# Kernel tuning notes

Hardware: AMD Instinct MI355X
Metric: run time of the kernel (lower is better)

## Reference

```python
import jax, jax.numpy as jnp
import numpy as np

B, S, SE, D, H = 4, 1024, 256, 1536, 24
HD = D // H
EPS = 1e-5
STYLE_IDX = np.array([0, 0, 2, 2])  # expand_first: style stats of sample 0 -> {0,1}, sample 2 -> {2,3}


def adain(feat):
    # feat: [B,H,S,hd]; stats over seq dim (-2), unbiased var like torch
    m = feat.mean(axis=-2, keepdims=True)
    s = jnp.sqrt(feat.var(axis=-2, keepdims=True, ddof=1) + EPS)
    sm, ss = m[STYLE_IDX], s[STYLE_IDX]
    styled = (feat - m) / s * ss + sm
    # only batch indices 1 and 3 are restyled
    mask = jnp.array([0.0, 1.0, 0.0, 1.0], dtype=feat.dtype).reshape(B, 1, 1, 1)
    return feat * (1.0 - mask) + styled * mask


def heads(x):
    b, s, _ = x.shape
    return x.reshape(b, s, H, HD).transpose(0, 2, 1, 3)


def setup_inputs() -> dict:
    key = jax.random.key(0)
    ks = jax.random.split(key, 12)
    w = lambda k: jax.random.normal(k, (D, D), dtype=jnp.float32) * 0.02
    z = jnp.zeros((D,), dtype=jnp.float32)
    return {
        'hidden_states': jax.random.normal(ks[0], (B, S, D), dtype=jnp.float32),
        'encoder_hidden_states': jax.random.normal(ks[1], (B, SE, D), dtype=jnp.float32),
        'wq': w(ks[2]), 'bq': z, 'wk': w(ks[3]), 'bk': z, 'wv': w(ks[4]), 'bv': z,
        'awq': w(ks[5]), 'abq': z, 'awk': w(ks[6]), 'abk': z, 'awv': w(ks[7]), 'abv': z,
        'wo': w(ks[8]), 'bo': z, 'wao': w(ks[9]), 'bao': z,
    }


def reference(hidden_states, encoder_hidden_states, wq, bq, wk, bk, wv, bv,
              awq, abq, awk, abk, awv, abv, wo, bo, wao, bao):
    q = heads(hidden_states @ wq + bq)   # [B,H,S,hd]
    k = heads(hidden_states @ wk + bk)
    v = heads(hidden_states @ wv + bv)
    # adain_queries / adain_keys (adain_values=False)
    q = adain(q)
    k = adain(k)
    # share_attention: concat style K/V (scale=1.0 -> plain expand) along seq
    k = jnp.concatenate([k, k[STYLE_IDX]], axis=2)  # [B,H,2S,hd]
    v = jnp.concatenate([v, v[STYLE_IDX]], axis=2)
    # joint (text) streams
    eq = heads(encoder_hidden_states @ awq + abq)
    ek = heads(encoder_hidden_states @ awk + abk)
    ev = heads(encoder_hidden_states @ awv + abv)
    q = jnp.concatenate([q, eq], axis=2)   # [B,H,S+SE,hd]
    k = jnp.concatenate([k, ek], axis=2)   # [B,H,2S+SE,hd]
    v = jnp.concatenate([v, ev], axis=2)
    scale = 1.0 / np.sqrt(HD)
    logits = jnp.einsum('bhqd,bhkd->bhqk', q, k) * scale
    probs = jax.nn.softmax(logits, axis=-1)
    out = jnp.einsum('bhqk,bhkd->bhqd', probs, v)
    out = out.transpose(0, 2, 1, 3).reshape(B, -1, D)
    hid, enc = out[:, :S], out[:, S:]
    hid = hid @ wo + bo            # to_out[0] (to_out[1] is dropout/identity)
    enc = enc @ wao + bao          # to_add_out (context_pre_only=False)
    return hid, enc
```

## Files before the change

### kernel.cpp

```cpp
#include <hip/hip_runtime.h>
#include <hip/hip_bf16.h>


#define NB 4
#define NS 1024
#define NSE 256
#define ND 1536
#define NH 24
#define LK2 1280
#define SMAX 20.0f
#define LOG2E 1.44269504f

typedef short bf16x8 __attribute__((ext_vector_type(8)));
typedef float f32x4 __attribute__((ext_vector_type(4)));

struct WPtrs { const float* w[8]; };
struct B6    { const float* p[6]; };

__device__ __forceinline__ unsigned short f2bf(float x) {
  union { float f; unsigned u; } a; a.f = x;
  unsigned r = a.u + 0x7fffu + ((a.u >> 16) & 1u);
  return (unsigned short)(r >> 16);
}
__device__ __forceinline__ void split2(float x, unsigned short& h, unsigned short& l) {
  union { float f; unsigned u; } a; a.f = x;
  h = (unsigned short)(a.u >> 16);
  union { float f; unsigned u; } b; b.u = a.u & 0xffff0000u;
  union { float f; unsigned u; } c; c.f = x - b.f;
  l = (unsigned short)(c.u >> 16);
}

__device__ __forceinline__ void gload_lds16(const unsigned short* g, unsigned short* l) {
  __builtin_amdgcn_global_load_lds(
      (const __attribute__((address_space(1))) void*)g,
      (__attribute__((address_space(3))) void*)l, 16, 0, 0);
}

__global__ __launch_bounds__(256) void conv_split_all(
    const float* __restrict__ hs, const float* __restrict__ ehs,
    unsigned short* __restrict__ HSh, unsigned short* __restrict__ HSl,
    unsigned short* __restrict__ EHh, unsigned short* __restrict__ EHl)
{
  int i = blockIdx.x * 256 + threadIdx.x;
  const float4* src; ushort4 *dh, *dl; int j;
  if (i < 1572864) { src = (const float4*)hs; j = i; dh = (ushort4*)HSh; dl = (ushort4*)HSl; }
  else { j = i - 1572864; src = (const float4*)ehs; dh = (ushort4*)EHh; dl = (ushort4*)EHl; }
  float4 v = src[j];
  ushort4 h, lo;
  split2(v.x, h.x, lo.x); split2(v.y, h.y, lo.y);
  split2(v.z, h.z, lo.z); split2(v.w, h.w, lo.w);
  dh[j] = h; dl[j] = lo;
}

__global__ __launch_bounds__(256) void conv_wt_all(WPtrs wp,
                                                   unsigned short* __restrict__ Wsp)
{
  __shared__ float tile[32][33];
  const int z = blockIdx.z;
  const float* W = wp.w[z];
  unsigned short* Th = Wsp + (long)(2 * z) * 2359296;
  unsigned short* Tl = Th + 2359296;
  const int k0 = blockIdx.x * 32, n0 = blockIdx.y * 32;
  const int r = threadIdx.x >> 5, c = threadIdx.x & 31;
#pragma unroll
  for (int i = 0; i < 4; ++i)
    tile[r + 8 * i][c] = W[(long)(k0 + r + 8 * i) * ND + n0 + c];
  __syncthreads();
#pragma unroll
  for (int i = 0; i < 4; ++i) {
    float v = tile[c][r + 8 * i];
    long o = (long)(n0 + r + 8 * i) * ND + k0 + c;
    unsigned short h, l;
    split2(v, h, l);
    Th[o] = h; Tl[o] = l;
  }
}

__device__ __forceinline__ void gemm_mfma_body(
    const unsigned short* __restrict__ Ah, const unsigned short* __restrict__ Al,
    const unsigned short* __restrict__ Bh, const unsigned short* __restrict__ Bl,
    const float* __restrict__ bias, float* __restrict__ C, int m0, int n0,
    bool third)
{
  __shared__ unsigned short sAh[128 * 32], sAl[128 * 32];
  __shared__ unsigned short sBh[128 * 32], sBl[128 * 32];

  const int t = threadIdx.x;
  const int w = t >> 6, l = t & 63;

  const int lr = l >> 2;
  const int lc = (l & 3) * 8;

  const unsigned short* pAh = Ah + (long)(m0 + 32 * w + lr) * ND + lc;
  const unsigned short* pAl = Al + (long)(m0 + 32 * w + lr) * ND + lc;
  const unsigned short* pBh = Bh + (long)(n0 + 32 * w + lr) * ND + lc;
  const unsigned short* pBl = Bl + (long)(n0 + 32 * w + lr) * ND + lc;

  unsigned short* qAh0 = &sAh[(32 * w) * 32];
  unsigned short* qAh1 = &sAh[(32 * w + 16) * 32];
  unsigned short* qAl0 = &sAl[(32 * w) * 32];
  unsigned short* qAl1 = &sAl[(32 * w + 16) * 32];
  unsigned short* qBh0 = &sBh[(32 * w) * 32];
  unsigned short* qBh1 = &sBh[(32 * w + 16) * 32];
  unsigned short* qBl0 = &sBl[(32 * w) * 32];
  unsigned short* qBl1 = &sBl[(32 * w + 16) * 32];

  const int rowA = (w >> 1) * 64 + (l & 15);
  const int rowB = (w & 1) * 64 + (l & 15);
  const int ko = (l >> 4) * 8;

  f32x4 acc[4][4] = {};

  for (int k0 = 0; k0 < ND; k0 += 32) {
    gload_lds16(pAh, qAh0);
    gload_lds16(pAh + 16 * ND, qAh1);
    if (third) {
      gload_lds16(pAl, qAl0);
      gload_lds16(pAl + 16 * ND, qAl1);
    }
    gload_lds16(pBh, qBh0);
    gload_lds16(pBh + 16 * ND, qBh1);
    gload_lds16(pBl, qBl0);
    gload_lds16(pBl + 16 * ND, qBl1);
    pAh += 32; pAl += 32; pBh += 32; pBl += 32;
    __syncthreads();

    bf16x8 fah[4], fal[4], fbh[4], fbl[4];
#pragma unroll
    for (int mt = 0; mt < 4; ++mt)
      fah[mt] = *(const bf16x8*)&sAh[(rowA + mt * 16) * 32 + ko];
    if (third) {
#pragma unroll
      for (int mt = 0; mt < 4; ++mt)
        fal[mt] = *(const bf16x8*)&sAl[(rowA + mt * 16) * 32 + ko];
    }
#pragma unroll
    for (int nt = 0; nt < 4; ++nt) {
      fbh[nt] = *(const bf16x8*)&sBh[(rowB + nt * 16) * 32 + ko];
      fbl[nt] = *(const bf16x8*)&sBl[(rowB + nt * 16) * 32 + ko];
    }
#pragma unroll
    for (int mt = 0; mt < 4; ++mt)
#pragma unroll
      for (int nt = 0; nt < 4; ++nt) {
        acc[mt][nt] = __builtin_amdgcn_mfma_f32_16x16x32_bf16(fah[mt], fbh[nt], acc[mt][nt], 0, 0, 0);
        acc[mt][nt] = __builtin_amdgcn_mfma_f32_16x16x32_bf16(fah[mt], fbl[nt], acc[mt][nt], 0, 0, 0);
      }
    if (third) {
#pragma unroll
      for (int mt = 0; mt < 4; ++mt)
#pragma unroll
        for (int nt = 0; nt < 4; ++nt)
          acc[mt][nt] = __builtin_amdgcn_mfma_f32_16x16x32_bf16(fal[mt], fbh[nt], acc[mt][nt], 0, 0, 0);
    }
    __syncthreads();
  }

  const int col0 = n0 + (w & 1) * 64 + (l & 15);
  const int row0 = m0 + (w >> 1) * 64 + (l >> 4) * 4;
#pragma unroll
  for (int nt = 0; nt < 4; ++nt) {
    float bv = bias[col0 + nt * 16];
#pragma unroll
    for (int mt = 0; mt < 4; ++mt)
#pragma unroll
      for (int r = 0; r < 4; ++r)
        C[(long)(row0 + mt * 16 + r) * ND + col0 + nt * 16] = acc[mt][nt][r] + bv;
  }
}

__global__ __launch_bounds__(256) void gemm3_all(
    const unsigned short* __restrict__ HSh, const unsigned short* __restrict__ HSl,
    const unsigned short* __restrict__ EHh, const unsigned short* __restrict__ EHl,
    const unsigned short* __restrict__ Wsp, B6 biases,
    float* __restrict__ Qb, float* __restrict__ EQb)
{
  const int z = blockIdx.z, y = blockIdx.y;
  const unsigned short *Ah, *Al;
  float* C;
  int m0, widx;
  if (y < 32) { Ah = HSh; Al = HSl; m0 = y * 128; widx = z;
                C = Qb + (long)z * 6291456; }
  else        { Ah = EHh; Al = EHl; m0 = (y - 32) * 128; widx = 3 + z;
                C = EQb + (long)z * 1572864; }
  const unsigned short* Bh = Wsp + (long)(2 * widx) * 2359296;
  const unsigned short* Bl = Bh + 2359296;
  gemm_mfma_body(Ah, Al, Bh, Bl, biases.p[widx], C, m0, blockIdx.x * 128,
                 z == 2);
}

__global__ __launch_bounds__(256) void gemm_out_all(
    const unsigned short* __restrict__ AOh,
    const unsigned short* __restrict__ Wsp,
    const float* __restrict__ bo, const float* __restrict__ bao,
    float* __restrict__ out)
{
  const int z = blockIdx.z, y = blockIdx.y;
  const unsigned short *Ah, *Bh, *Bl;
  const float* bias;
  float* C;
  int m0;
  if (y < 8) {
    Ah = AOh + (long)z * 1966080;
    m0 = y * 128;
    Bh = Wsp + (long)12 * 2359296; Bl = Bh + 2359296;
    bias = bo; C = out + (long)z * 1572864;
  } else {
    Ah = AOh + 1572864 + (long)z * 1966080;
    m0 = (y - 8) * 128;
    Bh = Wsp + (long)14 * 2359296; Bl = Bh + 2359296;
    bias = bao; C = out + 6291456 + (long)z * 393216;
  }
  gemm_mfma_body(Ah, Ah, Bh, Bl, bias, C, m0, blockIdx.x * 128, false);
}

__global__ __launch_bounds__(256) void adain_stats2(
    const float* __restrict__ Qb, const float* __restrict__ Kb,
    float* __restrict__ stm, float* __restrict__ sts,
    float* __restrict__ stm2, float* __restrict__ sts2)
{
  const float* X = blockIdx.z ? Kb : Qb;
  float* meanb = blockIdx.z ? stm2 : stm;
  float* sigb  = blockIdx.z ? sts2 : sts;
  const int b  = blockIdx.x;
  const int t  = threadIdx.x;
  const int dl = t & 63;
  const int sg = t >> 6;
  const int d  = blockIdx.y * 64 + dl;
  const float* xp = X + (long)b * NS * ND + d;
  float sum = 0.f, sq = 0.f;
  for (int s = sg; s < NS; s += 4) {
    float v = xp[(long)s * ND];
    sum += v; sq += v * v;
  }
  __shared__ float ss[4][64], s2[4][64];
  ss[sg][dl] = sum; s2[sg][dl] = sq;
  __syncthreads();
  if (t < 64) {
    float tot = ss[0][t] + ss[1][t] + ss[2][t] + ss[3][t];
    float tq  = s2[0][t] + s2[1][t] + s2[2][t] + s2[3][t];
    float mean = tot * (1.f / 1024.f);
    float var  = (tq - tot * mean) * (1.f / 1023.f);
    meanb[b * ND + blockIdx.y * 64 + t] = mean;
    sigb [b * ND + blockIdx.y * 64 + t] = sqrtf(var + 1e-5f);
  }
}

__global__ __launch_bounds__(256) void conv_KV(
    const float* __restrict__ Kf, const float* __restrict__ EKf,
    const float* __restrict__ Vf, const float* __restrict__ EVf,
    const float* __restrict__ stm2, const float* __restrict__ sts2,
    unsigned short* __restrict__ Kh, unsigned short* __restrict__ Kl,
    unsigned short* __restrict__ VT)
{
  __shared__ float tile[64][65];
  const int bh = blockIdx.y, b = bh / NH, h = bh - b * NH;
  if (blockIdx.x < 20) {
    const int key = blockIdx.x * 64 + (threadIdx.x >> 2);
    const int dc = (threadIdx.x & 3) * 16;
    const bool kad = ((b & 1) != 0) && (key < NS);
    const int srcb = b & 2;
    const float* src = (key < NS)
        ? Kf  + ((long)b * NS + key) * ND + h * 64 + dc
        : EKf + ((long)b * NSE + key - NS) * ND + h * 64 + dc;
    unsigned short* dh = Kh + ((long)bh * LK2 + key) * 64 + dc;
    unsigned short* dl = Kl + ((long)bh * LK2 + key) * 64 + dc;
    const long sb = (long)b * ND + h * 64 + dc;
    const long ss = (long)srcb * ND + h * 64 + dc;
#pragma unroll
    for (int i = 0; i < 4; ++i) {
      float4 v = *(const float4*)(src + 4 * i);
      if (kad) {
        float4 mb = *(const float4*)(stm2 + sb + 4 * i);
        float4 gb = *(const float4*)(sts2 + sb + 4 * i);
        float4 ms = *(const float4*)(stm2 + ss + 4 * i);
        float4 gs = *(const float4*)(sts2 + ss + 4 * i);
        v.x = (v.x - mb.x) * (gs.x / gb.x) + ms.x;
        v.y = (v.y - mb.y) * (gs.y / gb.y) + ms.y;
        v.z = (v.z - mb.z) * (gs.z / gb.z) + ms.z;
        v.w = (v.w - mb.w) * (gs.w / gb.w) + ms.w;
      }
      ushort4 hi, lo;
      split2(v.x, hi.x, lo.x); split2(v.y, hi.y, lo.y);
      split2(v.z, hi.z, lo.z); split2(v.w, hi.w, lo.w);
      *(ushort4*)(dh + 4 * i) = hi;
      *(ushort4*)(dl + 4 * i) = lo;
    }
  } else {
    const int k0 = (blockIdx.x - 20) * 64;
    {
      const int kl_ = threadIdx.x >> 2, dc = (threadIdx.x & 3) * 16;
      const int key = k0 + kl_;
      const float* src = (key < NS)
          ? Vf  + ((long)b * NS + key) * ND + h * 64 + dc
          : EVf + ((long)b * NSE + key - NS) * ND + h * 64 + dc;
#pragma unroll
      for (int i = 0; i < 4; ++i) {
        float4 v = *(const float4*)(src + 4 * i);
        tile[kl_][dc + 4 * i + 0] = v.x; tile[kl_][dc + 4 * i + 1] = v.y;
        tile[kl_][dc + 4 * i + 2] = v.z; tile[kl_][dc + 4 * i + 3] = v.w;
      }
    }
    __syncthreads();
    const int d = threadIdx.x >> 2, kc = (threadIdx.x & 3) * 16;
    unsigned short* dst = VT + ((long)bh * 64 + d) * LK2 + k0 + kc;
#pragma unroll
    for (int i = 0; i < 4; ++i) {
      ushort4 o4;
      o4.x = f2bf(tile[kc + 4 * i + 0][d]);
      o4.y = f2bf(tile[kc + 4 * i + 1][d]);
      o4.z = f2bf(tile[kc + 4 * i + 2][d]);
      o4.w = f2bf(tile[kc + 4 * i + 3][d]);
      *(ushort4*)(dst + 4 * i) = o4;
    }
  }
}

__global__ __launch_bounds__(256) void attn_mfma(
    const float* __restrict__ Q, const float* __restrict__ EQ,
    const unsigned short* __restrict__ Khg, const unsigned short* __restrict__ Klg,
    const unsigned short* __restrict__ VTg,
    const float* __restrict__ stm, const float* __restrict__ sts,
    unsigned short* __restrict__ AOh)
{
  __shared__ unsigned short sKh[2][64 * 64], sKl[2][64 * 64], sVT[2][64 * 64];
  __shared__ unsigned short sPh[64 * 72], sPl[64 * 72];

  const int t = threadIdx.x, w = t >> 6, l = t & 63;
  const int lin = blockIdx.x;
  const int x = lin & 7;
  const int j = lin >> 3;
  const int parity = j & 1;
  const int u = j >> 1;
  const int i6 = 6 * x + u / 20;
  const int q0 = (u % 20) * 64;
  const int bh = parity ? (i6 < 24 ? i6 + 24 : i6 + 48)
                        : (i6 < 24 ? i6      : i6 + 24);
  const int b = bh / NH, h = bh - b * NH;
  const int bhs = (b & 2) * NH + h;
  const int m = l & 15, g = l >> 4;
  const bool beven = (b & 1) == 0;
  const int nIter = beven ? 20 : 36;

  union FU { bf16x8 v; unsigned short u[8]; };
  FU qh[2], ql[2];
  {
    const bool qad = !beven && (q0 < NS);
    const int srcb = b & 2;
    const float* qrow = (q0 < NS)
        ? (Q  + ((long)b * NS + q0 + 16 * w + m) * ND + h * 64)
        : (EQ + ((long)b * NSE + (q0 - NS) + 16 * w + m) * ND + h * 64);
#pragma unroll
    for (int ks = 0; ks < 2; ++ks) {
      const int d0 = h * 64 + ks * 32 + g * 8;
      const float* p = qrow + ks * 32 + g * 8;
      float4 v0 = *(const float4*)p, v1 = *(const float4*)(p + 4);
      float vv[8] = {v0.x, v0.y, v0.z, v0.w, v1.x, v1.y, v1.z, v1.w};
      if (qad) {
        float4 mb0 = *(const float4*)(stm + (long)b * ND + d0);
        float4 mb1 = *(const float4*)(stm + (long)b * ND + d0 + 4);
        float4 gb0 = *(const float4*)(sts + (long)b * ND + d0);
        float4 gb1 = *(const float4*)(sts + (long)b * ND + d0 + 4);
        float4 ms0 = *(const float4*)(stm + (long)srcb * ND + d0);
        float4 ms1 = *(const float4*)(stm + (long)srcb * ND + d0 + 4);
        float4 gs0 = *(const float4*)(sts + (long)srcb * ND + d0);
        float4 gs1 = *(const float4*)(sts + (long)srcb * ND + d0 + 4);
        float mb[8] = {mb0.x, mb0.y, mb0.z, mb0.w, mb1.x, mb1.y, mb1.z, mb1.w};
        float gb[8] = {gb0.x, gb0.y, gb0.z, gb0.w, gb1.x, gb1.y, gb1.z, gb1.w};
        float ms[8] = {ms0.x, ms0.y, ms0.z, ms0.w, ms1.x, ms1.y, ms1.z, ms1.w};
        float gs[8] = {gs0.x, gs0.y, gs0.z, gs0.w, gs1.x, gs1.y, gs1.z, gs1.w};
#pragma unroll
        for (int j2 = 0; j2 < 8; ++j2)
          vv[j2] = (vv[j2] - mb[j2]) * (gs[j2] / gb[j2]) + ms[j2];
      }
#pragma unroll
      for (int j2 = 0; j2 < 8; ++j2)
        split2(vv[j2] * (0.125f * LOG2E), qh[ks].u[j2], ql[ks].u[j2]);
    }
  }

  const int srow = l >> 3;
  const int sp = l & 7;
  const int osw = (sp - srow) & 7;
  const long ownK = (long)bh * LK2 * 64, styK = (long)bhs * LK2 * 64;
  const long ownV = (long)bh * 64 * LK2, styV = (long)bhs * 64 * LK2;
  const int offK = (16 * w + srow) * 64 + osw * 8;
  const int offV = (16 * w + srow) * LK2 + osw * 8;

  auto stage = [&](int kt, int bi) {
    int zone, jz;
    if (beven) { zone = (kt < 16) ? 0 : 2; jz = (kt < 16) ? kt : kt - 16; }
    else {
      zone = (kt < 16) ? 0 : ((kt < 32) ? 1 : 2);
      jz = (kt < 16) ? kt : ((kt < 32) ? kt - 16 : kt - 32);
    }
    const long keyBase = ((zone == 2) ? 1024 : 0) + (long)jz * 64;
    const unsigned short* kb = Khg + ((zone == 1) ? styK : ownK) + keyBase * 64;
    const unsigned short* lb = Klg + ((zone == 1) ? styK : ownK) + keyBase * 64;
    const unsigned short* vb = VTg + ((zone == 1) ? styV : ownV) + keyBase;
    gload_lds16(kb + offK, &sKh[bi][(16 * w) * 64]);
    gload_lds16(kb + 8 * 64 + offK, &sKh[bi][(16 * w + 8) * 64]);
    gload_lds16(lb + offK, &sKl[bi][(16 * w) * 64]);
    gload_lds16(lb + 8 * 64 + offK, &sKl[bi][(16 * w + 8) * 64]);
    gload_lds16(vb + offV, &sVT[bi][(16 * w) * 64]);
    gload_lds16(vb + 8 * LK2 + offV, &sVT[bi][(16 * w + 8) * 64]);
  };

  const int p0 = (g + m) & 7;
  const int p1 = (4 + g + m) & 7;

  f32x4 oacc[4] = {};
  float l_part[4] = {0.f, 0.f, 0.f, 0.f};

  stage(0, 0);

  for (int kt = 0; kt < nIter; ++kt) {
    const int cur = kt & 1;
    __syncthreads();
    if (kt + 1 < nIter) stage(kt + 1, cur ^ 1);

    const float ebias = (beven && kt < 16) ? (1.0f - SMAX * LOG2E)
                                           : (-SMAX * LOG2E);

    f32x4 sacc[4] = {};
    __builtin_amdgcn_s_setprio(1);
#pragma unroll
    for (int ks = 0; ks < 2; ++ks) {
      const int pp = ks ? p1 : p0;
#pragma unroll
      for (int nt = 0; nt < 4; ++nt) {
        const int ak = (nt * 16 + m) * 64 + pp * 8;
        bf16x8 fkh = *(const bf16x8*)&sKh[cur][ak];
        bf16x8 fkl = *(const bf16x8*)&sKl[cur][ak];
        sacc[nt] = __builtin_amdgcn_mfma_f32_16x16x32_bf16(qh[ks].v, fkh, sacc[nt], 0, 0, 0);
        sacc[nt] = __builtin_amdgcn_mfma_f32_16x16x32_bf16(qh[ks].v, fkl, sacc[nt], 0, 0, 0);
        sacc[nt] = __builtin_amdgcn_mfma_f32_16x16x32_bf16(ql[ks].v, fkh, sacc[nt], 0, 0, 0);
      }
    }
    __builtin_amdgcn_s_setprio(0);

#pragma unroll
    for (int nt = 0; nt < 4; ++nt)
#pragma unroll
      for (int r = 0; r < 4; ++r)
        sacc[nt][r] = __builtin_amdgcn_exp2f(sacc[nt][r] + ebias);
#pragma unroll
    for (int r = 0; r < 4; ++r)
      l_part[r] += (sacc[0][r] + sacc[1][r]) + (sacc[2][r] + sacc[3][r]);
#pragma unroll
    for (int nt = 0; nt < 4; ++nt)
#pragma unroll
      for (int r = 0; r < 4; ++r) {
        unsigned short ph, pl;
        split2(sacc[nt][r], ph, pl);
        const int ad = (16 * w + 4 * g + r) * 72 + nt * 16 + m;
        sPh[ad] = ph; sPl[ad] = pl;
      }

    __builtin_amdgcn_s_setprio(1);
#pragma unroll
    for (int ks = 0; ks < 2; ++ks) {
      const int pp = ks ? p1 : p0;
      const int ap = (16 * w + m) * 72 + ks * 32 + g * 8;
      bf16x8 fph = *(const bf16x8*)&sPh[ap];
      bf16x8 fpl = *(const bf16x8*)&sPl[ap];
#pragma unroll
      for (int nt2 = 0; nt2 < 4; ++nt2) {
        const int av = (nt2 * 16 + m) * 64 + pp * 8;
        bf16x8 fv = *(const bf16x8*)&sVT[cur][av];
        oacc[nt2] = __builtin_amdgcn_mfma_f32_16x16x32_bf16(fph, fv, oacc[nt2], 0, 0, 0);
        oacc[nt2] = __builtin_amdgcn_mfma_f32_16x16x32_bf16(fpl, fv, oacc[nt2], 0, 0, 0);
      }
    }
    __builtin_amdgcn_s_setprio(0);
  }

#pragma unroll
  for (int r = 0; r < 4; ++r) {
#pragma unroll
    for (int off = 1; off < 16; off <<= 1)
      l_part[r] += __shfl_xor(l_part[r], off, 16);
  }
#pragma unroll
  for (int r = 0; r < 4; ++r) {
    float inv = 1.f / l_part[r];
    const long row = (long)b * 1280 + q0 + 16 * w + 4 * g + r;
    const long base = row * ND + h * 64;
#pragma unroll
    for (int nt2 = 0; nt2 < 4; ++nt2)
      AOh[base + nt2 * 16 + m] = f2bf(oacc[nt2][r] * inv);
  }
}

extern "C" void kernel_launch(void* const* d_in, const int* in_sizes, int n_in,
                              void* d_out, int out_size, void* d_ws, size_t ws_size,
                              hipStream_t stream) {
  const float* hs  = (const float*)d_in[0];
  const float* ehs = (const float*)d_in[1];
  WPtrs wp;
  wp.w[0] = (const float*)d_in[2];  wp.w[1] = (const float*)d_in[4];
  wp.w[2] = (const float*)d_in[6];  wp.w[3] = (const float*)d_in[8];
  wp.w[4] = (const float*)d_in[10]; wp.w[5] = (const float*)d_in[12];
  wp.w[6] = (const float*)d_in[14]; wp.w[7] = (const float*)d_in[16];
  B6 biases;
  biases.p[0] = (const float*)d_in[3];
  biases.p[1] = (const float*)d_in[5];
  biases.p[2] = (const float*)d_in[7];
  biases.p[3] = (const float*)d_in[9];
  biases.p[4] = (const float*)d_in[11];
  biases.p[5] = (const float*)d_in[13];
  const float* bo  = (const float*)d_in[15];
  const float* bao = (const float*)d_in[17];
  float* out = (float*)d_out;

  float* Qb  = (float*)d_ws;
  float* Kb  = Qb  + 6291456;
  float* Vb  = Kb  + 6291456;
  float* EQb = Vb  + 6291456;
  float* EKb = EQb + 1572864;
  float* EVb = EKb + 1572864;
  float* stm  = EVb + 1572864;
  float* sts  = stm + 6144;
  float* stm2 = sts + 6144;
  float* sts2 = stm2 + 6144;
  unsigned short* U0  = (unsigned short*)(sts2 + 6144);
  unsigned short* HSh = U0;
  unsigned short* HSl = U0 + 6291456;
  unsigned short* EHh = U0 + 12582912;
  unsigned short* EHl = U0 + 14155776;
  unsigned short* AOh = U0;
  unsigned short* Wsp = U0 + 15728640;
  unsigned short* Khg = Wsp;
  unsigned short* Klg = Wsp + 7864320;
  unsigned short* VTg = Wsp + 15728640;

  dim3 blk(256);

  conv_split_all<<<7680, blk, 0, stream>>>(hs, ehs, HSh, HSl, EHh, EHl);
  conv_wt_all<<<dim3(48, 48, 8), blk, 0, stream>>>(wp, Wsp);

  gemm3_all<<<dim3(12, 40, 3), blk, 0, stream>>>(
      HSh, HSl, EHh, EHl, Wsp, biases, Qb, EQb);

  adain_stats2<<<dim3(4, 24, 2), blk, 0, stream>>>(Qb, Kb, stm, sts, stm2, sts2);

  conv_KV<<<dim3(40, 96), blk, 0, stream>>>(Kb, EKb, Vb, EVb, stm2, sts2,
                                            Khg, Klg, VTg);

  attn_mfma<<<dim3(1920), blk, 0, stream>>>(Qb, EQb, Khg, Klg, VTg,
                                            stm, sts, AOh);

  gemm_out_all<<<dim3(12, 10, 4), blk, 0, stream>>>(AOh, Wsp, bo, bao, out);
}
```

Baseline: 759.9 us.

## Halve attention key tile, pair even/odd heads per block, raise occupancy

The attention kernel now stages 32-key tiles instead of 64, which roughly halves shared memory per block, and sets launch bounds to 4 blocks per CU to raise occupancy. Each block now processes two (batch, head) segments in turn, one even batch with 40 iterations and one odd batch with 72, so all blocks carry the same amount of work and the grid is halved. A new swizzle for the transposed V tile and a narrower P buffer go with the smaller tile. In exchange there are twice as many iterations and barriers per key range, and less MFMA work between each barrier.

```diff
diff --git a/kernel.cpp b/kernel.cpp
--- a/kernel.cpp
+++ b/kernel.cpp
@@ -316,179 +316,177 @@
   }
 }
 
-__global__ __launch_bounds__(256) void attn_mfma(
+__global__ __launch_bounds__(256, 4) void attn_mfma(
     const float* __restrict__ Q, const float* __restrict__ EQ,
     const unsigned short* __restrict__ Khg, const unsigned short* __restrict__ Klg,
     const unsigned short* __restrict__ VTg,
     const float* __restrict__ stm, const float* __restrict__ sts,
     unsigned short* __restrict__ AOh)
 {
-  __shared__ unsigned short sKh[2][64 * 64], sKl[2][64 * 64], sVT[2][64 * 64];
-  __shared__ unsigned short sPh[64 * 72], sPl[64 * 72];
+  __shared__ unsigned short sKh[2][32 * 64], sKl[2][32 * 64], sVT[2][64 * 32];
+  __shared__ unsigned short sPh[64 * 40], sPl[64 * 40];
 
   const int t = threadIdx.x, w = t >> 6, l = t & 63;
-  const int lin = blockIdx.x;
-  const int x = lin & 7;
-  const int j = lin >> 3;
-  const int parity = j & 1;
-  const int u = j >> 1;
+  const int x = blockIdx.x & 7;
+  const int u = blockIdx.x >> 3;
   const int i6 = 6 * x + u / 20;
   const int q0 = (u % 20) * 64;
-  const int bh = parity ? (i6 < 24 ? i6 + 24 : i6 + 48)
-                        : (i6 < 24 ? i6      : i6 + 24);
-  const int b = bh / NH, h = bh - b * NH;
-  const int bhs = (b & 2) * NH + h;
   const int m = l & 15, g = l >> 4;
-  const bool beven = (b & 1) == 0;
-  const int nIter = beven ? 20 : 36;
-
-  union FU { bf16x8 v; unsigned short u[8]; };
-  FU qh[2], ql[2];
-  {
-    const bool qad = !beven && (q0 < NS);
-    const int srcb = b & 2;
-    const float* qrow = (q0 < NS)
-        ? (Q  + ((long)b * NS + q0 + 16 * w + m) * ND + h * 64)
-        : (EQ + ((long)b * NSE + (q0 - NS) + 16 * w + m) * ND + h * 64);
-#pragma unroll
-    for (int ks = 0; ks < 2; ++ks) {
-      const int d0 = h * 64 + ks * 32 + g * 8;
-      const float* p = qrow + ks * 32 + g * 8;
-      float4 v0 = *(const float4*)p, v1 = *(const float4*)(p + 4);
-      float vv[8] = {v0.x, v0.y, v0.z, v0.w, v1.x, v1.y, v1.z, v1.w};
-      if (qad) {
-        float4 mb0 = *(const float4*)(stm + (long)b * ND + d0);
-        float4 mb1 = *(const float4*)(stm + (long)b * ND + d0 + 4);
-        float4 gb0 = *(const float4*)(sts + (long)b * ND + d0);
-        float4 gb1 = *(const float4*)(sts + (long)b * ND + d0 + 4);
-        float4 ms0 = *(const float4*)(stm + (long)srcb * ND + d0);
-        float4 ms1 = *(const float4*)(stm + (long)srcb * ND + d0 + 4);
-        float4 gs0 = *(const float4*)(sts + (long)srcb * ND + d0);
-        float4 gs1 = *(const float4*)(sts + (long)srcb * ND + d0 + 4);
-        float mb[8] = {mb0.x, mb0.y, mb0.z, mb0.w, mb1.x, mb1.y, mb1.z, mb1.w};
-        float gb[8] = {gb0.x, gb0.y, gb0.z, gb0.w, gb1.x, gb1.y, gb1.z, gb1.w};
-        float ms[8] = {ms0.x, ms0.y, ms0.z, ms0.w, ms1.x, ms1.y, ms1.z, ms1.w};
-        float gs[8] = {gs0.x, gs0.y, gs0.z, gs0.w, gs1.x, gs1.y, gs1.z, gs1.w};
-#pragma unroll
-        for (int j2 = 0; j2 < 8; ++j2)
-          vv[j2] = (vv[j2] - mb[j2]) * (gs[j2] / gb[j2]) + ms[j2];
-      }
-#pragma unroll
-      for (int j2 = 0; j2 < 8; ++j2)
-        split2(vv[j2] * (0.125f * LOG2E), qh[ks].u[j2], ql[ks].u[j2]);
-    }
-  }
-
-  const int srow = l >> 3;
-  const int sp = l & 7;
-  const int osw = (sp - srow) & 7;
-  const long ownK = (long)bh * LK2 * 64, styK = (long)bhs * LK2 * 64;
-  const long ownV = (long)bh * 64 * LK2, styV = (long)bhs * 64 * LK2;
-  const int offK = (16 * w + srow) * 64 + osw * 8;
-  const int offV = (16 * w + srow) * LK2 + osw * 8;
-
-  auto stage = [&](int kt, int bi) {
-    int zone, jz;
-    if (beven) { zone = (kt < 16) ? 0 : 2; jz = (kt < 16) ? kt : kt - 16; }
-    else {
-      zone = (kt < 16) ? 0 : ((kt < 32) ? 1 : 2);
-      jz = (kt < 16) ? kt : ((kt < 32) ? kt - 16 : kt - 32);
-    }
-    const long keyBase = ((zone == 2) ? 1024 : 0) + (long)jz * 64;
-    const unsigned short* kb = Khg + ((zone == 1) ? styK : ownK) + keyBase * 64;
-    const unsigned short* lb = Klg + ((zone == 1) ? styK : ownK) + keyBase * 64;
-    const unsigned short* vb = VTg + ((zone == 1) ? styV : ownV) + keyBase;
-    gload_lds16(kb + offK, &sKh[bi][(16 * w) * 64]);
-    gload_lds16(kb + 8 * 64 + offK, &sKh[bi][(16 * w + 8) * 64]);
-    gload_lds16(lb + offK, &sKl[bi][(16 * w) * 64]);
-    gload_lds16(lb + 8 * 64 + offK, &sKl[bi][(16 * w + 8) * 64]);
-    gload_lds16(vb + offV, &sVT[bi][(16 * w) * 64]);
-    gload_lds16(vb + 8 * LK2 + offV, &sVT[bi][(16 * w + 8) * 64]);
-  };
+
+  const int srow = l >> 3, sp = l & 7;
+  const int offK = (8 * w + srow) * 64 + ((sp - srow) & 7) * 8;
+  const int dv = l >> 2, cv = l & 3;
+  const int vrow = 16 * w + dv;
+  const int vcol = ((cv - ((dv + (dv >> 2)) & 3)) & 3) * 8;
+  const int rfm = (m + (m >> 2)) & 3;
 
   const int p0 = (g + m) & 7;
   const int p1 = (4 + g + m) & 7;
 
-  f32x4 oacc[4] = {};
-  float l_part[4] = {0.f, 0.f, 0.f, 0.f};
-
-  stage(0, 0);
-
-  for (int kt = 0; kt < nIter; ++kt) {
-    const int cur = kt & 1;
-    __syncthreads();
-    if (kt + 1 < nIter) stage(kt + 1, cur ^ 1);
-
-    const float ebias = (beven && kt < 16) ? (1.0f - SMAX * LOG2E)
-                                           : (-SMAX * LOG2E);
-
-    f32x4 sacc[4] = {};
-    __builtin_amdgcn_s_setprio(1);
-#pragma unroll
-    for (int ks = 0; ks < 2; ++ks) {
-      const int pp = ks ? p1 : p0;
-#pragma unroll
-      for (int nt = 0; nt < 4; ++nt) {
-        const int ak = (nt * 16 + m) * 64 + pp * 8;
-        bf16x8 fkh = *(const bf16x8*)&sKh[cur][ak];
-        bf16x8 fkl = *(const bf16x8*)&sKl[cur][ak];
-        sacc[nt] = __builtin_amdgcn_mfma_f32_16x16x32_bf16(qh[ks].v, fkh, sacc[nt], 0, 0, 0);
-        sacc[nt] = __builtin_amdgcn_mfma_f32_16x16x32_bf16(qh[ks].v, fkl, sacc[nt], 0, 0, 0);
-        sacc[nt] = __builtin_amdgcn_mfma_f32_16x16x32_bf16(ql[ks].v, fkh, sacc[nt], 0, 0, 0);
-      }
-    }
-    __builtin_amdgcn_s_setprio(0);
-
-#pragma unroll
-    for (int nt = 0; nt < 4; ++nt)
+  union FU { bf16x8 v; unsigned short u[8]; };
+
+  for (int seg = 0; seg < 2; ++seg) {
+    const int bh = seg ? (i6 < 24 ? i6 + 24 : i6 + 48)
+                       : (i6 < 24 ? i6      : i6 + 24);
+    const int b = bh / NH, h = bh - b * NH;
+    const int bhs = (b & 2) * NH + h;
+    const bool beven = (seg == 0);
+    const int nIter = beven ? 40 : 72;
+
+    FU qh[2], ql[2];
+    {
+      const bool qad = !beven && (q0 < NS);
+      const int srcb = b & 2;
+      const float* qrow = (q0 < NS)
+          ? (Q  + ((long)b * NS + q0 + 16 * w + m) * ND + h * 64)
+          : (EQ + ((long)b * NSE + (q0 - NS) + 16 * w + m) * ND + h * 64);
+#pragma unroll
+      for (int ks = 0; ks < 2; ++ks) {
+        const int d0 = h * 64 + ks * 32 + g * 8;
+        const float* p = qrow + ks * 32 + g * 8;
+        float4 v0 = *(const float4*)p, v1 = *(const float4*)(p + 4);
+        float vv[8] = {v0.x, v0.y, v0.z, v0.w, v1.x, v1.y, v1.z, v1.w};
+        if (qad) {
+          float4 mb0 = *(const float4*)(stm + (long)b * ND + d0);
+          float4 mb1 = *(const float4*)(stm + (long)b * ND + d0 + 4);
+          float4 gb0 = *(const float4*)(sts + (long)b * ND + d0);
+          float4 gb1 = *(const float4*)(sts + (long)b * ND + d0 + 4);
+          float4 ms0 = *(const float4*)(stm + (long)srcb * ND + d0);
+          float4 ms1 = *(const float4*)(stm + (long)srcb * ND + d0 + 4);
+          float4 gs0 = *(const float4*)(sts + (long)srcb * ND + d0);
+          float4 gs1 = *(const float4*)(sts + (long)srcb * ND + d0 + 4);
+          float mb[8] = {mb0.x, mb0.y, mb0.z, mb0.w, mb1.x, mb1.y, mb1.z, mb1.w};
+          float gb[8] = {gb0.x, gb0.y, gb0.z, gb0.w, gb1.x, gb1.y, gb1.z, gb1.w};
+          float ms[8] = {ms0.x, ms0.y, ms0.z, ms0.w, ms1.x, ms1.y, ms1.z, ms1.w};
+          float gs[8] = {gs0.x, gs0.y, gs0.z, gs0.w, gs1.x, gs1.y, gs1.z, gs1.w};
+#pragma unroll
+          for (int j2 = 0; j2 < 8; ++j2)
+            vv[j2] = (vv[j2] - mb[j2]) * (gs[j2] / gb[j2]) + ms[j2];
+        }
+#pragma unroll
+        for (int j2 = 0; j2 < 8; ++j2)
+          split2(vv[j2] * (0.125f * LOG2E), qh[ks].u[j2], ql[ks].u[j2]);
+      }
+    }
+
+    const long ownK = (long)bh * LK2 * 64, styK = (long)bhs * LK2 * 64;
+    const long ownV = (long)bh * 64 * LK2, styV = (long)bhs * 64 * LK2;
+
+    auto stage = [&](int kt, int bi) {
+      int zone, jz;
+      if (beven) { zone = (kt < 32) ? 0 : 2; jz = (kt < 32) ? kt : kt - 32; }
+      else {
+        zone = (kt < 32) ? 0 : ((kt < 64) ? 1 : 2);
+        jz = (kt < 32) ? kt : ((kt < 64) ? kt - 32 : kt - 64);
+      }
+      const long keyBase = ((zone == 2) ? 1024 : 0) + (long)jz * 32;
+      const unsigned short* kb = Khg + ((zone == 1) ? styK : ownK) + keyBase * 64;
+      const unsigned short* lb = Klg + ((zone == 1) ? styK : ownK) + keyBase * 64;
+      const unsigned short* vb = VTg + ((zone == 1) ? styV : ownV) + keyBase;
+      gload_lds16(kb + offK, &sKh[bi][(8 * w) * 64]);
+      gload_lds16(lb + offK, &sKl[bi][(8 * w) * 64]);
+      gload_lds16(vb + (long)vrow * LK2 + vcol, &sVT[bi][(16 * w) * 32]);
+    };
+
+    f32x4 oacc[4] = {};
+    float l_part[4] = {0.f, 0.f, 0.f, 0.f};
+
+    stage(0, 0);
+
+    for (int kt = 0; kt < nIter; ++kt) {
+      const int cur = kt & 1;
+      __syncthreads();
+      if (kt + 1 < nIter) stage(kt + 1, cur ^ 1);
+
+      const float ebias = (beven && kt < 32) ? (1.0f - SMAX * LOG2E)
+                                             : (-SMAX * LOG2E);
+
+      f32x4 sacc[2] = {};
+      __builtin_amdgcn_s_setprio(1);
+#pragma unroll
+      for (int ks = 0; ks < 2; ++ks) {
+        const int pp = ks ? p1 : p0;
+#pragma unroll
+        for (int nt = 0; nt < 2; ++nt) {
+          const int ak = (nt * 16 + m) * 64 + pp * 8;
+          bf16x8 fkh = *(const bf16x8*)&sKh[cur][ak];
+          bf16x8 fkl = *(const bf16x8*)&sKl[cur][ak];
+          sacc[nt] = __builtin_amdgcn_mfma_f32_16x16x32_bf16(qh[ks].v, fkh, sacc[nt], 0, 0, 0);
+          sacc[nt] = __builtin_amdgcn_mfma_f32_16x16x32_bf16(qh[ks].v, fkl, sacc[nt], 0, 0, 0);
+          sacc[nt] = __builtin_amdgcn_mfma_f32_16x16x32_bf16(ql[ks].v, fkh, sacc[nt], 0, 0, 0);
+        }
+      }
+      __builtin_amdgcn_s_setprio(0);
+
+#pragma unroll
+      for (int nt = 0; nt < 2; ++nt)
+#pragma unroll
+        for (int r = 0; r < 4; ++r)
+          sacc[nt][r] = __builtin_amdgcn_exp2f(sacc[nt][r] + ebias);
 #pragma unroll
       for (int r = 0; r < 4; ++r)
-        sacc[nt][r] = __builtin_amdgcn_exp2f(sacc[nt][r] + ebias);
-#pragma unroll
-    for (int r = 0; r < 4; ++r)
-      l_part[r] += (sacc[0][r] + sacc[1][r]) + (sacc[2][r] + sacc[3][r]);
-#pragma unroll
-    for (int nt = 0; nt < 4; ++nt)
-#pragma unroll
-      for (int r = 0; r < 4; ++r) {
-        unsigned short ph, pl;
-        split2(sacc[nt][r], ph, pl);
-        const int ad = (16 * w + 4 * g + r) * 72 + nt * 16 + m;
-        sPh[ad] = ph; sPl[ad] = pl;
-      }
-
-    __builtin_amdgcn_s_setprio(1);
-#pragma unroll
-    for (int ks = 0; ks < 2; ++ks) {
-      const int pp = ks ? p1 : p0;
-      const int ap = (16 * w + m) * 72 + ks * 32 + g * 8;
-      bf16x8 fph = *(const bf16x8*)&sPh[ap];
-      bf16x8 fpl = *(const bf16x8*)&sPl[ap];
-#pragma unroll
-      for (int nt2 = 0; nt2 < 4; ++nt2) {
-        const int av = (nt2 * 16 + m) * 64 + pp * 8;
-        bf16x8 fv = *(const bf16x8*)&sVT[cur][av];
-        oacc[nt2] = __builtin_amdgcn_mfma_f32_16x16x32_bf16(fph, fv, oacc[nt2], 0, 0, 0);
-        oacc[nt2] = __builtin_amdgcn_mfma_f32_16x16x32_bf16(fpl, fv, oacc[nt2], 0, 0, 0);
-      }
-    }
-    __builtin_amdgcn_s_setprio(0);
-  }
-
-#pragma unroll
-  for (int r = 0; r < 4; ++r) {
-#pragma unroll
-    for (int off = 1; off < 16; off <<= 1)
-      l_part[r] += __shfl_xor(l_part[r], off, 16);
-  }
-#pragma unroll
-  for (int r = 0; r < 4; ++r) {
-    float inv = 1.f / l_part[r];
-    const long row = (long)b * 1280 + q0 + 16 * w + 4 * g + r;
-    const long base = row * ND + h * 64;
-#pragma unroll
-    for (int nt2 = 0; nt2 < 4; ++nt2)
-      AOh[base + nt2 * 16 + m] = f2bf(oacc[nt2][r] * inv);
+        l_part[r] += sacc[0][r] + sacc[1][r];
+#pragma unroll
+      for (int nt = 0; nt < 2; ++nt)
+#pragma unroll
+        for (int r = 0; r < 4; ++r) {
+          unsigned short ph, pl;
+          split2(sacc[nt][r], ph, pl);
+          const int ad = (16 * w + 4 * g + r) * 40 + nt * 16 + m;
+          sPh[ad] = ph; sPl[ad] = pl;
+        }
+
+      __builtin_amdgcn_s_setprio(1);
+      {
+        const int ap = (16 * w + m) * 40 + g * 8;
+        bf16x8 fph = *(const bf16x8*)&sPh[ap];
+        bf16x8 fpl = *(const bf16x8*)&sPl[ap];
+#pragma unroll
+        for (int nt2 = 0; nt2 < 4; ++nt2) {
+          const int av = (nt2 * 16 + m) * 32 + ((g + rfm) & 3) * 8;
+          bf16x8 fv = *(const bf16x8*)&sVT[cur][av];
+          oacc[nt2] = __builtin_amdgcn_mfma_f32_16x16x32_bf16(fph, fv, oacc[nt2], 0, 0, 0);
+          oacc[nt2] = __builtin_amdgcn_mfma_f32_16x16x32_bf16(fpl, fv, oacc[nt2], 0, 0, 0);
+        }
+      }
+      __builtin_amdgcn_s_setprio(0);
+    }
+
+#pragma unroll
+    for (int r = 0; r < 4; ++r) {
+#pragma unroll
+      for (int off = 1; off < 16; off <<= 1)
+        l_part[r] += __shfl_xor(l_part[r], off, 16);
+    }
+#pragma unroll
+    for (int r = 0; r < 4; ++r) {
+      float inv = 1.f / l_part[r];
+      const long row = (long)b * 1280 + q0 + 16 * w + 4 * g + r;
+      const long base = row * ND + h * 64;
+#pragma unroll
+      for (int nt2 = 0; nt2 < 4; ++nt2)
+        AOh[base + nt2 * 16 + m] = f2bf(oacc[nt2][r] * inv);
+    }
   }
 }
 
@@ -547,8 +545,8 @@
   conv_KV<<<dim3(40, 96), blk, 0, stream>>>(Kb, EKb, Vb, EVb, stm2, sts2,
                                             Khg, Klg, VTg);
 
-  attn_mfma<<<dim3(1920), blk, 0, stream>>>(Qb, EQb, Khg, Klg, VTg,
-                                            stm, sts, AOh);
+  attn_mfma<<<dim3(960), blk, 0, stream>>>(Qb, EQb, Khg, Klg, VTg,
+                                           stm, sts, AOh);
 
   gemm_out_all<<<dim3(12, 10, 4), blk, 0, stream>>>(AOh, Wsp, bo, bao, out);
 }
```

Result: faster. 695.9 us (-8.4%).
